# Optimization experiments

Measured on AMD Instinct MI355X. Metric: run time of the kernel, lower is better.

## Reference

```python
import jax, jax.numpy as jnp
import numpy as np

REACH = 3  # neighborhood reach -> 24 causal neighbors, 48 MLP input features


def setup_inputs() -> dict:
    key = jax.random.key(0)
    ks = jax.random.split(key, 5)
    b, c, h, w = 8, 3, 192, 192
    x = jax.random.uniform(ks[0], (b, c, h, w), dtype=jnp.float32)

    def lin(k, fi, fo):
        k1, k2 = jax.random.split(k)
        s = 1.0 / np.sqrt(fi).astype(np.float32)
        W = jax.random.uniform(k1, (fi, fo), minval=-s, maxval=s, dtype=jnp.float32)
        bias = jax.random.uniform(k2, (fo,), minval=-s, maxval=s, dtype=jnp.float32)
        return W, bias

    W1, b1 = lin(ks[1], 48, 96)
    W2, b2 = lin(ks[2], 96, 24)
    W3, b3 = lin(ks[3], 24, 12)
    W4, b4 = lin(ks[4], 12, 1)
    return dict(x=x, W1=W1, b1=b1, W2=W2, b2=b2, W3=W3, b3=b3, W4=W4, b4=b4)


def _forward(x, W1, b1, W2, b2, W3, b3, W4, b4):
    b, c, h, w = x.shape
    r = REACH
    H2, Wd = h - 2 * r, w - 2 * r  # interior grid of predicted pixels

    # Precompute the 24 image-neighborhood taps for every interior pixel.
    # Order matches torch get_nb: 3 rows above (7 cols each, row-major), then 3 cols left.
    slabs = [x[:, :, dy:dy + H2, dx:dx + Wd] for dy in range(r) for dx in range(2 * r + 1)]
    slabs += [x[:, :, r:r + H2, dx:dx + Wd] for dx in range(r)]
    xnb = jnp.transpose(jnp.stack(slabs, axis=-1), (2, 3, 0, 1, 4))   # (H2, Wd, b, c, 24)
    xtgt = jnp.transpose(x[:, :, r:r + H2, r:r + Wd], (2, 3, 0, 1))    # (H2, Wd, b, c)

    def mlp(f):  # f: (b, c, 48)
        f = jnp.tanh(f @ W1 + b1)
        f = jnp.tanh(f @ W2 + b2)
        f = jnp.tanh(f @ W3 + b3)
        f = jnp.tanh(f @ W4 + b4)
        return f[..., 0]  # (b, c)

    def row_step(prev3, row_xs):
        # prev3: (b, c, 3, w) = last 3 full (zero-padded) delta rows
        xnb_row, xtgt_row = row_xs  # (Wd, b, c, 24), (Wd, b, c)
        # 21 delta taps from the 3 previous rows, vectorized over columns.
        pslabs = [prev3[:, :, dy, dx:dx + Wd] for dy in range(r) for dx in range(2 * r + 1)]
        pnb = jnp.transpose(jnp.stack(pslabs, axis=-1), (2, 0, 1, 3))  # (Wd, b, c, 21)

        def col_step(last3, xs):
            # last3: (b, c, 3) = 3 most recent deltas in current row (zeros at row start)
            xn, pn, tgt = xs
            feat = jnp.concatenate([xn, pn, last3], axis=-1)  # (b, c, 48)
            delta = tgt - mlp(feat)
            last3 = jnp.concatenate([last3[:, :, 1:], delta[:, :, None]], axis=-1)
            return last3, delta

        last3_0 = jnp.zeros((b, c, r), x.dtype)
        _, row_d = jax.lax.scan(col_step, last3_0, (xnb_row, pnb, xtgt_row))  # (Wd, b, c)
        row_full = jnp.pad(jnp.transpose(row_d, (1, 2, 0)), ((0, 0), (0, 0), (r, w - r - Wd)))
        prev3 = jnp.concatenate([prev3[:, :, 1:, :], row_full[:, :, None, :]], axis=2)
        return prev3, row_d

    prev3_0 = jnp.zeros((b, c, r, w), x.dtype)
    _, all_d = jax.lax.scan(row_step, prev3_0, (xnb, xtgt))  # (H2, Wd, b, c)

    # torch averages square(deltas) over the full (b, c, h-2, w) buffer, whose
    # only nonzeros are the (H2, Wd) interior deltas.
    total = b * c * (h - 2) * w
    return jnp.sqrt(jnp.sum(all_d * all_d) / total)


def reference(x, W1, b1, W2, b2, W3, b3, W4, b4):
    return _forward(x, W1, b1, W2, b2, W3, b3, W4, b4)
```

## Files before the change

kernel.cpp:

```cpp
#include <hip/hip_runtime.h>

#define NPLANES 24
#define IMG 192
#define RW 194
#define GRID2 186
#define NPIX (GRID2 * GRID2)
#define SLACK 6
#define TSTEPS (926 + 11 * SLACK)

typedef _Float16 f16x8 __attribute__((ext_vector_type(8)));
typedef _Float16 h2v   __attribute__((ext_vector_type(2)));
typedef float    f32x4 __attribute__((ext_vector_type(4)));
typedef __fp16   fp16x2 __attribute__((ext_vector_type(2)));

__device__ float PreBuf[(unsigned long long)NPLANES * NPIX * 100];

__device__ __forceinline__ h2v pk(float a, float b) {
  union { fp16x2 p; h2v h; } u;
  u.p = __builtin_amdgcn_cvt_pkrtz(a, b);
  return u.h;
}
__device__ __forceinline__ unsigned pkn(float a, float b) {
  union { _Float16 h[2]; unsigned u; } x;
  x.h[0] = (_Float16)a; x.h[1] = (_Float16)b;
  return x.u;
}
__device__ __forceinline__ float fast_tanh(float x) {
  float e = __builtin_amdgcn_exp2f(x * 2.885390081777927f);
  return __builtin_fmaf(-2.0f, __builtin_amdgcn_rcpf(e + 1.0f), 1.0f);
}

__launch_bounds__(192)
__global__ void prepass_kernel(const float* __restrict__ x,
                               const float* __restrict__ W1g,
                               const float* __restrict__ b1g)
{
  __shared__ float xs[4][IMG];
  const int tid = threadIdx.x;
  const int plane = blockIdx.x / GRID2;
  const int a = blockIdx.x - plane * GRID2;
  const float* __restrict__ xp = x + (size_t)plane * (IMG * IMG) + (size_t)a * IMG;
  #pragma unroll
  for (int r = 0; r < 4; ++r) xs[r][tid] = xp[r * IMG + tid];
  __syncthreads();
  if (tid >= GRID2) return;

  float f[24];
  #pragma unroll
  for (int dy = 0; dy < 3; ++dy)
    #pragma unroll
    for (int dx = 0; dx < 7; ++dx) f[7 * dy + dx] = xs[dy][tid + dx];
  #pragma unroll
  for (int dx = 0; dx < 3; ++dx) f[21 + dx] = xs[3][tid + dx];

  float acc[96];
  #pragma unroll
  for (int n = 0; n < 96; ++n) acc[n] = b1g[n];
  #pragma unroll
  for (int k = 0; k < 24; ++k) {
    const float fk = f[k];
    const float* __restrict__ wr = W1g + k * 96;
    #pragma unroll
    for (int n = 0; n < 96; ++n) acc[n] = fmaf(fk, wr[n], acc[n]);
  }

  float* op = PreBuf + (size_t)(plane * NPIX + a * GRID2 + tid) * 100;
  #pragma unroll
  for (int g = 0; g < 4; ++g)
    #pragma unroll
    for (int nt = 0; nt < 6; ++nt) {
      float4 st;
      st.x = acc[32 * (nt >> 1) + 8 * g + 4 * (nt & 1) + 0];
      st.y = acc[32 * (nt >> 1) + 8 * g + 4 * (nt & 1) + 1];
      st.z = acc[32 * (nt >> 1) + 8 * g + 4 * (nt & 1) + 2];
      st.w = acc[32 * (nt >> 1) + 8 * g + 4 * (nt & 1) + 3];
      *(float4*)(op + g * 24 + nt * 4) = st;
    }
  op[96] = xs[3][tid + 3];
}

__launch_bounds__(192)
__global__ void codec_kernel(const float* __restrict__ x,
                             const float* __restrict__ W1g, const float* __restrict__ b1g,
                             const float* __restrict__ W2g, const float* __restrict__ b2g,
                             const float* __restrict__ W3g, const float* __restrict__ b3g,
                             const float* __restrict__ W4g, const float* __restrict__ b4g,
                             float* __restrict__ ws)
{
  __shared__ __align__(16) _Float16 ringH[64 * RW];
  __shared__ int   ctrL[4];
  __shared__ float wsum[3];

  const int tid  = threadIdx.x;
  const int lane = tid & 63;
  const int w    = __builtin_amdgcn_readfirstlane(tid >> 6);
  const int lam  = lane & 15;
  const int quad = lane >> 4;
  const int cell = 16 * w + lam;
  const float* __restrict__ pre = PreBuf + (size_t)blockIdx.x * NPIX * 100;
  (void)x; (void)b1g;

  { unsigned* z = (unsigned*)ringH; for (int u = tid; u < 64 * RW / 2; u += 192) z[u] = 0; }
  if (tid < 4) ctrL[tid] = -1;

  f16x8 A1s[6];
  #pragma unroll
  for (int nt = 0; nt < 6; ++nt) {
    union { _Float16 h[8]; f16x8 v; } u;
    const int n1 = 32 * (nt >> 1) + 8 * (lam >> 2) + 4 * (nt & 1) + (lam & 3);
    #pragma unroll
    for (int e = 0; e < 8; ++e) {
      float v = 0.f;
      if (quad == 0) {
        if (e < 2) v = W1g[(46 - e) * 96 + n1];
      } else if (quad == 1) {
        if (e < 6) v = W1g[(38 + e) * 96 + n1];
      } else if (e < 7) {
        v = W1g[(24 + 7 * (3 - quad) + e) * 96 + n1];
      }
      u.h[e] = (_Float16)v;
    }
    A1s[nt] = u.v;
  }
  f16x8 A1f[6];
  #pragma unroll
  for (int nt = 0; nt < 6; ++nt) {
    union { _Float16 h[8]; f16x8 v; } u;
    const int n1 = 32 * (nt >> 1) + 8 * (lam >> 2) + 4 * (nt & 1) + (lam & 3);
    #pragma unroll
    for (int e = 0; e < 8; ++e) {
      float v = 0.f;
      if (quad == 0 && e < 2) v = W1g[((e == 0) ? 44 : 47) * 96 + n1];
      u.h[e] = (_Float16)v;
    }
    A1f[nt] = u.v;
  }
  f16x8 A2[2][3];
  #pragma unroll
  for (int mt = 0; mt < 2; ++mt) {
    const int n2 = 8 * (lam >> 2) + 4 * mt + (lam & 3);
    #pragma unroll
    for (int kt = 0; kt < 3; ++kt) {
      union { _Float16 h[8]; f16x8 v; } u;
      #pragma unroll
      for (int e = 0; e < 8; ++e) {
        const int k2 = 32 * kt + 8 * quad + e;
        u.h[e] = (n2 < 24) ? (_Float16)W2g[k2 * 24 + n2] : (_Float16)0.f;
      }
      A2[mt][kt] = u.v;
    }
  }
  f16x8 A3;
  { union { _Float16 h[8]; f16x8 v; } u;
    #pragma unroll
    for (int e = 0; e < 8; ++e) {
      const int k3 = 8 * quad + e;
      u.h[e] = (k3 < 24 && lam < 12) ? (_Float16)W3g[k3 * 12 + lam] : (_Float16)0.f;
    }
    A3 = u.v; }
  f16x8 A4;
  { union { _Float16 h[8]; f16x8 v; } u;
    #pragma unroll
    for (int e = 0; e < 8; ++e) {
      const int m = 4 * quad + e;
      u.h[e] = ((lam & 3) == 0 && e < 4 && m < 12) ? (_Float16)W4g[m] : (_Float16)0.f;
    }
    A4 = u.v; }

  f32x4 b2q[2], b3q, b4q;
  #pragma unroll
  for (int mt = 0; mt < 2; ++mt)
    #pragma unroll
    for (int r = 0; r < 4; ++r) {
      const int n2 = 8 * quad + 4 * mt + r;
      b2q[mt][r] = (n2 < 24) ? b2g[n2] : 0.f;
    }
  #pragma unroll
  for (int r = 0; r < 4; ++r)
    b3q[r] = (4 * quad + r < 12) ? b3g[4 * quad + r] : 0.f;
  { const float b4v = b4g[0]; b4q[0] = b4v; b4q[1] = b4v; b4q[2] = b4v; b4q[3] = b4v; }

  __syncthreads();

  const int prodw = (w == 0) ? 2 : w - 1;
  const unsigned flagRA = (unsigned)(size_t)&ctrL[prodw];
  const unsigned flagWA = (unsigned)(size_t)&ctrL[w];
  const unsigned* ru32 = (const unsigned*)ringH;
  const unsigned short* rhu = (const unsigned short*)ringH;

  int i  = cell;
  int jj = -(4 * cell + SLACK * w);
  unsigned dl1g = 0, dl2g = 0;
  unsigned bfx0 = 0;
  float sumsq = 0.f, xtA = 0.f, xtB = 0.f;
  f32x4 SA[6], SB[6], PreP[6];
  #pragma unroll
  for (int q = 0; q < 6; ++q) {
    SA[q] = (f32x4){0.f,0.f,0.f,0.f};
    SB[q] = (f32x4){0.f,0.f,0.f,0.f};
    PreP[q] = (f32x4){0.f,0.f,0.f,0.f};
  }

  {
    if (jj >= 0 && i <= 185) {
      const float* pp = pre + (size_t)(i * GRID2 + jj) * 100;
      const f32x4* pv = (const f32x4*)(pp + quad * 24);
      #pragma unroll
      for (int q = 0; q < 6; ++q) PreP[q] = pv[q];
      xtA = pp[96];
    }
    const int rq = quad ? quad : 3;
    const int e0 = jj & ~1;
    const int dwi = ((i - rq) & 63) * 97 + (e0 >> 1);
    const unsigned w0 = ru32[dwi], w1 = ru32[dwi + 1];
    const unsigned w2 = ru32[dwi + 2], w3 = ru32[dwi + 3];
    const bool odd = jj & 1;
    const unsigned a01 = (w0 >> 16) | (w1 << 16);
    const unsigned a12 = (w1 >> 16) | (w2 << 16);
    const unsigned a23 = (w2 >> 16) | (w3 << 16);
    const unsigned t0 = odd ? a01 : w0, t1 = odd ? a12 : w1;
    const unsigned t2 = odd ? a23 : w2, t3 = odd ? (w3 >> 16) : w3;
    union { unsigned u[4]; f16x8 v; } bs;
    bs.u[0] = quad ? t0 : 0u;
    bs.u[1] = quad ? t1 : 0u;
    bs.u[2] = quad ? t2 : 0u;
    bs.u[3] = quad ? t3 : 0u;
    #pragma unroll
    for (int nt = 0; nt < 6; ++nt)
      SA[nt] = __builtin_amdgcn_mfma_f32_16x16x32_f16(A1s[nt], bs.v, PreP[nt], 0, 0, 0);
  }

#define SUBSTEP(T, SC, SN, XTC, XTN)                                            \
  {                                                                             \
    int _cv;                                                                    \
    asm volatile("ds_read_b32 %0, %1" : "=v"(_cv) : "v"(flagRA));               \
    const bool _act = (jj >= 0) && (i <= 185);                                  \
    const int _cb = 3 + jj;                                                     \
    int _iN = i, _jN = jj + 1;                                                  \
    if (_jN > 185) { _iN += 48; _jN -= 192 + 3 * SLACK; }                       \
                       \
    const int _rq = quad ? quad : 3;                                            \
    const int _e0 = _jN & ~1;                                                   \
    const int _dwi = ((_iN - _rq) & 63) * 97 + (_e0 >> 1);                      \
    const unsigned _w0 = ru32[_dwi],     _w1 = ru32[_dwi + 1];                  \
    const unsigned _w2 = ru32[_dwi + 2], _w3 = ru32[_dwi + 3];                  \
    const unsigned short _lf = rhu[((_iN - 1) & 63) * RW + (_jN + 6)];          \
    const unsigned _q0d = dl1g | (dl2g << 16);                                  \
    if (_jN >= 0 && _iN <= 185) {                                               \
      const float* _pp = pre + (size_t)(_iN * GRID2 + _jN) * 100;               \
      const f32x4* _pv = (const f32x4*)(_pp + quad * 24);                       \
      PreP[0]=_pv[0]; PreP[1]=_pv[1]; PreP[2]=_pv[2];                           \
      PreP[3]=_pv[3]; PreP[4]=_pv[4]; PreP[5]=_pv[5];                           \
      XTN = _pp[96];                                                            \
    }                                                                           \
                                      \
    union { unsigned u[4]; f16x8 v; } _bfx;                                     \
    _bfx.u[0] = bfx0; _bfx.u[1] = 0u; _bfx.u[2] = 0u; _bfx.u[3] = 0u;           \
    f32x4 _h1a[6];                                                              \
    _Pragma("unroll")                                                           \
    for (int nt = 0; nt < 6; ++nt)                                              \
      _h1a[nt] = __builtin_amdgcn_mfma_f32_16x16x32_f16(A1f[nt], _bfx.v, SC[nt], 0, 0, 0); \
    f16x8 _B2f[3];                                                              \
    _Pragma("unroll")                                                           \
    for (int kt = 0; kt < 3; ++kt) {                                            \
      union { h2v p[4]; f16x8 v; } _u;                                          \
      _u.p[0] = pk(fast_tanh(_h1a[2*kt][0]), fast_tanh(_h1a[2*kt][1]));         \
      _u.p[1] = pk(fast_tanh(_h1a[2*kt][2]), fast_tanh(_h1a[2*kt][3]));         \
      _u.p[2] = pk(fast_tanh(_h1a[2*kt+1][0]), fast_tanh(_h1a[2*kt+1][1]));     \
      _u.p[3] = pk(fast_tanh(_h1a[2*kt+1][2]), fast_tanh(_h1a[2*kt+1][3]));     \
      _B2f[kt] = _u.v;                                                          \
    }                                                                           \
    f32x4 _a20 = b2q[0], _a21 = b2q[1];                                         \
    _a20 = __builtin_amdgcn_mfma_f32_16x16x32_f16(A2[0][0], _B2f[0], _a20, 0, 0, 0); \
    _a20 = __builtin_amdgcn_mfma_f32_16x16x32_f16(A2[0][1], _B2f[1], _a20, 0, 0, 0); \
    _a20 = __builtin_amdgcn_mfma_f32_16x16x32_f16(A2[0][2], _B2f[2], _a20, 0, 0, 0); \
    _a21 = __builtin_amdgcn_mfma_f32_16x16x32_f16(A2[1][0], _B2f[0], _a21, 0, 0, 0); \
    _a21 = __builtin_amdgcn_mfma_f32_16x16x32_f16(A2[1][1], _B2f[1], _a21, 0, 0, 0); \
    _a21 = __builtin_amdgcn_mfma_f32_16x16x32_f16(A2[1][2], _B2f[2], _a21, 0, 0, 0); \
    f16x8 _B3f;                                                                 \
    { union { h2v p[4]; f16x8 v; } _u;                                          \
      _u.p[0] = pk(fast_tanh(_a20[0]), fast_tanh(_a20[1]));                     \
      _u.p[1] = pk(fast_tanh(_a20[2]), fast_tanh(_a20[3]));                     \
      _u.p[2] = pk(fast_tanh(_a21[0]), fast_tanh(_a21[1]));                     \
      _u.p[3] = pk(fast_tanh(_a21[2]), fast_tanh(_a21[3]));                     \
      _B3f = _u.v; }                                                            \
    f32x4 _a3 = __builtin_amdgcn_mfma_f32_16x16x32_f16(A3, _B3f, b3q, 0, 0, 0); \
    f16x8 _B4f;                                                                 \
    { union { unsigned u[4]; f16x8 v; } _u;                                     \
      union { h2v p; unsigned s; } _p0, _p1;                                    \
      _p0.p = pk(fast_tanh(_a3[0]), fast_tanh(_a3[1]));                         \
      _p1.p = pk(fast_tanh(_a3[2]), fast_tanh(_a3[3]));                         \
      _u.u[0] = _p0.s; _u.u[1] = _p1.s; _u.u[2] = 0u; _u.u[3] = 0u;             \
      _B4f = _u.v; }                                                            \
    const f32x4 _a4 = __builtin_amdgcn_mfma_f32_16x16x32_f16(A4, _B4f, b4q, 0, 0, 0); \
    const float _pred = fast_tanh(_a4[0]);                                      \
    const float _d = XTC - _pred;                                               \
    const float _de = _act ? _d : 0.f;                                          \
    if (quad == 0) sumsq += _de * _de;                                          \
    if (quad == 0 && _act) ringH[(i & 63) * RW + _cb] = (_Float16)_de;          \
             \
    { union { float f; int b; } _dc; _dc.f = _de;                               \
      int _si = __builtin_amdgcn_update_dpp(0, _dc.b, 0x111, 0xF, 0xF, false);  \
      union { int b; float f; } _sc; _sc.b = _si;                               \
      float _fr = _sc.f;                                                        \
      union { unsigned short s; _Float16 h; } _lh; _lh.s = _lf;                 \
      if (lam == 0) _fr = (float)_lh.h;                                         \
      if (_jN + 3 > 185) _fr = 0.f;                                             \
      bfx0 = (quad == 0) ? pkn(_fr, _de) : 0u; }                                \
                                \
    { union { _Float16 h; unsigned short s; } _dh; _dh.h = (_Float16)_de;       \
      if (_act) {                                                               \
        if (jj == 185) { dl1g = 0; dl2g = 0; }                                  \
        else { dl2g = dl1g; dl1g = (unsigned)_dh.s; }                           \
      } }                                                                       \
                                            \
    { const bool _odd = _jN & 1;                                                \
      const unsigned _a01 = (_w0 >> 16) | (_w1 << 16);                          \
      const unsigned _a12 = (_w1 >> 16) | (_w2 << 16);                          \
      const unsigned _a23 = (_w2 >> 16) | (_w3 << 16);                          \
      const unsigned _t0 = _odd ? _a01 : _w0, _t1 = _odd ? _a12 : _w1;          \
      const unsigned _t2 = _odd ? _a23 : _w2, _t3 = _odd ? (_w3 >> 16) : _w3;   \
      union { unsigned u[4]; f16x8 v; } _bs;                                    \
      _bs.u[0] = quad ? _t0 : _q0d;                                             \
      _bs.u[1] = quad ? _t1 : 0u;                                               \
      _bs.u[2] = quad ? _t2 : 0u;                                               \
      _bs.u[3] = quad ? _t3 : 0u;                                               \
      _Pragma("unroll")                                                         \
      for (int nt = 0; nt < 6; ++nt)                                            \
        SN[nt] = __builtin_amdgcn_mfma_f32_16x16x32_f16(A1s[nt], _bs.v, PreP[nt], 0, 0, 0); \
    }                                                                           \
        \
    if (lane == 0)                                                              \
      asm volatile("s_waitcnt lgkmcnt(0)\n\tds_write_b32 %0, %1"                \
                   :: "v"(flagWA), "v"(T) : "memory");                          \
    asm volatile("s_waitcnt lgkmcnt(0)" : "+v"(_cv) :: "memory");               \
    if (_cv < (T) - (SLACK - 1)) {                                              \
      int _g = 0;                                                               \
      do { __builtin_amdgcn_s_sleep(2);                                         \
           _cv = __hip_atomic_load(&ctrL[prodw], __ATOMIC_ACQUIRE,              \
                                   __HIP_MEMORY_SCOPE_WORKGROUP);               \
      } while (_cv < (T) - (SLACK - 1) && ++_g < (1 << 22));                    \
    }                                                                           \
    asm volatile("" ::: "memory");                                              \
    i = _iN; jj = _jN;                                                          \
  }

  for (int t = 0; t < TSTEPS; t += 2) {
    SUBSTEP(t,     SA, SB, xtA, xtB);
    SUBSTEP(t + 1, SB, SA, xtB, xtA);
  }
#undef SUBSTEP

  #pragma unroll
  for (int off = 32; off >= 1; off >>= 1) sumsq += __shfl_down(sumsq, off);
  if (lane == 0) wsum[w] = sumsq;
  __syncthreads();
  if (tid == 0) ws[blockIdx.x] = wsum[0] + wsum[1] + wsum[2];
}

__global__ void finalize_kernel(const float* __restrict__ ws, float* __restrict__ out) {
  if (threadIdx.x == 0) {
    float s = 0.0f;
    #pragma unroll
    for (int p = 0; p < NPLANES; ++p) s += ws[p];
    out[0] = sqrtf(s / 875520.0f);
  }
}

extern "C" void kernel_launch(void* const* d_in, const int* in_sizes, int n_in,
                              void* d_out, int out_size, void* d_ws, size_t ws_size,
                              hipStream_t stream) {
  (void)in_sizes; (void)n_in; (void)out_size; (void)ws_size;
  const float* x  = (const float*)d_in[0];
  const float* W1 = (const float*)d_in[1];
  const float* b1 = (const float*)d_in[2];
  const float* W2 = (const float*)d_in[3];
  const float* b2 = (const float*)d_in[4];
  const float* W3 = (const float*)d_in[5];
  const float* b3 = (const float*)d_in[6];
  const float* W4 = (const float*)d_in[7];
  const float* b4 = (const float*)d_in[8];
  float* ws = (float*)d_ws;

  prepass_kernel<<<NPLANES * GRID2, 192, 0, stream>>>(x, W1, b1);
  codec_kernel<<<NPLANES, 192, 0, stream>>>(x, W1, b1, W2, b2, W3, b3, W4, b4, ws);
  finalize_kernel<<<1, 64, 0, stream>>>(ws, (float*)d_out);
}
```

Measured before the change: 1.235 ms.

## Pack two planes per block and use four waves per plane in codec

The sequential codec kernel now runs two image planes per workgroup, and each plane gets four wavefronts instead of three. Each wave still owns 16 rows in the wavefront-skewed schedule, so a pass now covers 64 rows and the row-wrap offsets are updated to match. This halves the number of workgroups and adds a wave per plane, keeping the total step count unchanged. The aim is more latency hiding per CU, at the cost of eight waves competing for the same CU's SIMDs and a longer producer–consumer chain per plane.

```diff
diff --git a/kernel.cpp b/kernel.cpp
--- a/kernel.cpp
+++ b/kernel.cpp
@@ -7,6 +7,10 @@
 #define NPIX (GRID2 * GRID2)
 #define SLACK 6
 #define TSTEPS (926 + 11 * SLACK)
+#define PPB 2
+#define WPP 4
+#define NTHR (PPB * WPP * 64)
+#define NBLK (NPLANES / PPB)
 
 typedef _Float16 f16x8 __attribute__((ext_vector_type(8)));
 typedef _Float16 h2v   __attribute__((ext_vector_type(2)));
@@ -79,7 +83,7 @@
   op[96] = xs[3][tid + 3];
 }
 
-__launch_bounds__(192)
+__launch_bounds__(NTHR)
 __global__ void codec_kernel(const float* __restrict__ x,
                              const float* __restrict__ W1g, const float* __restrict__ b1g,
                              const float* __restrict__ W2g, const float* __restrict__ b2g,
@@ -87,21 +91,26 @@
                              const float* __restrict__ W4g, const float* __restrict__ b4g,
                              float* __restrict__ ws)
 {
-  __shared__ __align__(16) _Float16 ringH[64 * RW];
-  __shared__ int   ctrL[4];
-  __shared__ float wsum[3];
+  __shared__ __align__(16) _Float16 ringS[PPB][64 * RW];
+  __shared__ int   ctrL[PPB][4];
+  __shared__ float wsum[PPB][WPP];
 
   const int tid  = threadIdx.x;
   const int lane = tid & 63;
-  const int w    = __builtin_amdgcn_readfirstlane(tid >> 6);
+  const int Wv   = __builtin_amdgcn_readfirstlane(tid >> 6);
+  const int pl   = Wv >> 2;
+  const int w    = Wv & 3;
   const int lam  = lane & 15;
   const int quad = lane >> 4;
   const int cell = 16 * w + lam;
-  const float* __restrict__ pre = PreBuf + (size_t)blockIdx.x * NPIX * 100;
+  const int ptid = tid & (NTHR / PPB - 1);
+  const int plane = blockIdx.x * PPB + pl;
+  const float* __restrict__ pre = PreBuf + (size_t)plane * NPIX * 100;
+  _Float16* __restrict__ ringH = ringS[pl];
   (void)x; (void)b1g;
 
-  { unsigned* z = (unsigned*)ringH; for (int u = tid; u < 64 * RW / 2; u += 192) z[u] = 0; }
-  if (tid < 4) ctrL[tid] = -1;
+  { unsigned* z = (unsigned*)ringH; for (int u = ptid; u < 64 * RW / 2; u += 256) z[u] = 0; }
+  if (ptid < 4) ctrL[pl][ptid] = -1;
 
   f16x8 A1s[6];
   #pragma unroll
@@ -182,11 +191,11 @@
 
   __syncthreads();
 
-  const int prodw = (w == 0) ? 2 : w - 1;
-  const unsigned flagRA = (unsigned)(size_t)&ctrL[prodw];
-  const unsigned flagWA = (unsigned)(size_t)&ctrL[w];
+  const unsigned flagRA = (unsigned)(size_t)&ctrL[pl][(w + 3) & 3];
+  const unsigned flagWA = (unsigned)(size_t)&ctrL[pl][w];
   const unsigned* ru32 = (const unsigned*)ringH;
   const unsigned short* rhu = (const unsigned short*)ringH;
+  int* const prodCtr = &ctrL[pl][(w + 3) & 3];
 
   int i  = cell;
   int jj = -(4 * cell + SLACK * w);
@@ -237,7 +246,7 @@
     const bool _act = (jj >= 0) && (i <= 185);                                  \
     const int _cb = 3 + jj;                                                     \
     int _iN = i, _jN = jj + 1;                                                  \
-    if (_jN > 185) { _iN += 48; _jN -= 192 + 3 * SLACK; }                       \
+    if (_jN > 185) { _iN += 64; _jN -= 256 + 4 * SLACK; }                       \
                        \
     const int _rq = quad ? quad : 3;                                            \
     const int _e0 = _jN & ~1;                                                   \
@@ -307,7 +316,7 @@
       if (lam == 0) _fr = (float)_lh.h;                                         \
       if (_jN + 3 > 185) _fr = 0.f;                                             \
       bfx0 = (quad == 0) ? pkn(_fr, _de) : 0u; }                                \
-                                \
+                                                            \
     { union { _Float16 h; unsigned short s; } _dh; _dh.h = (_Float16)_de;       \
       if (_act) {                                                               \
         if (jj == 185) { dl1g = 0; dl2g = 0; }                                  \
@@ -337,7 +346,7 @@
     if (_cv < (T) - (SLACK - 1)) {                                              \
       int _g = 0;                                                               \
       do { __builtin_amdgcn_s_sleep(2);                                         \
-           _cv = __hip_atomic_load(&ctrL[prodw], __ATOMIC_ACQUIRE,              \
+           _cv = __hip_atomic_load(prodCtr, __ATOMIC_ACQUIRE,                   \
                                    __HIP_MEMORY_SCOPE_WORKGROUP);               \
       } while (_cv < (T) - (SLACK - 1) && ++_g < (1 << 22));                    \
     }                                                                           \
@@ -353,9 +362,10 @@
 
   #pragma unroll
   for (int off = 32; off >= 1; off >>= 1) sumsq += __shfl_down(sumsq, off);
-  if (lane == 0) wsum[w] = sumsq;
+  if (lane == 0) wsum[pl][w] = sumsq;
   __syncthreads();
-  if (tid == 0) ws[blockIdx.x] = wsum[0] + wsum[1] + wsum[2];
+  if (ptid == 0)
+    ws[plane] = wsum[pl][0] + wsum[pl][1] + wsum[pl][2] + wsum[pl][3];
 }
 
 __global__ void finalize_kernel(const float* __restrict__ ws, float* __restrict__ out) {
@@ -383,6 +393,6 @@
   float* ws = (float*)d_ws;
 
   prepass_kernel<<<NPLANES * GRID2, 192, 0, stream>>>(x, W1, b1);
-  codec_kernel<<<NPLANES, 192, 0, stream>>>(x, W1, b1, W2, b2, W3, b3, W4, b4, ws);
+  codec_kernel<<<NBLK, NTHR, 0, stream>>>(x, W1, b1, W2, b2, W3, b3, W4, b4, ws);
   finalize_kernel<<<1, 64, 0, stream>>>(ws, (float*)d_out);
 }
```

After: 1.650 ms. 33.6% more time.

## Batch tanh reciprocals, reduce wavefront slack, and move progress flag after wait

Applied to the files above, without the earlier changes.

Adds a tanh4 helper that computes four tanh values with a single shared reciprocal, replacing four separate rcp ops per accumulator vector. The pipeline slack between producer and consumer waves drops from 6 to 4, which shortens the total step count. The progress-flag write now happens after the spin-wait instead of before it. That shortens the serial dependence chain, but it changes the publish ordering and can lose precision or overflow when the exp products are large.

```diff
diff --git a/kernel.cpp b/kernel.cpp
--- a/kernel.cpp
+++ b/kernel.cpp
@@ -5,7 +5,7 @@
 #define RW 194
 #define GRID2 186
 #define NPIX (GRID2 * GRID2)
-#define SLACK 6
+#define SLACK 4
 #define TSTEPS (926 + 11 * SLACK)
 
 typedef _Float16 f16x8 __attribute__((ext_vector_type(8)));
@@ -28,6 +28,22 @@
 __device__ __forceinline__ float fast_tanh(float x) {
   float e = __builtin_amdgcn_exp2f(x * 2.885390081777927f);
   return __builtin_fmaf(-2.0f, __builtin_amdgcn_rcpf(e + 1.0f), 1.0f);
+}
+__device__ __forceinline__ f32x4 tanh4(f32x4 x) {
+  const float K = 2.885390081777927f;
+  const float a0 = __builtin_amdgcn_exp2f(x[0] * K) + 1.0f;
+  const float a1 = __builtin_amdgcn_exp2f(x[1] * K) + 1.0f;
+  const float a2 = __builtin_amdgcn_exp2f(x[2] * K) + 1.0f;
+  const float a3 = __builtin_amdgcn_exp2f(x[3] * K) + 1.0f;
+  const float q01 = a0 * a1, q23 = a2 * a3;
+  const float r = __builtin_amdgcn_rcpf(q01 * q23);
+  const float r01 = r * q23, r23 = r * q01;
+  f32x4 o;
+  o[0] = __builtin_fmaf(-2.0f, r01 * a1, 1.0f);
+  o[1] = __builtin_fmaf(-2.0f, r01 * a0, 1.0f);
+  o[2] = __builtin_fmaf(-2.0f, r23 * a3, 1.0f);
+  o[3] = __builtin_fmaf(-2.0f, r23 * a2, 1.0f);
+  return o;
 }
 
 __launch_bounds__(192)
@@ -187,6 +203,7 @@
   const unsigned flagWA = (unsigned)(size_t)&ctrL[w];
   const unsigned* ru32 = (const unsigned*)ringH;
   const unsigned short* rhu = (const unsigned short*)ringH;
+  int* const prodCtr = &ctrL[prodw];
 
   int i  = cell;
   int jj = -(4 * cell + SLACK * w);
@@ -263,11 +280,13 @@
     f16x8 _B2f[3];                                                              \
     _Pragma("unroll")                                                           \
     for (int kt = 0; kt < 3; ++kt) {                                            \
+      const f32x4 _ta = tanh4(_h1a[2 * kt]);                                    \
+      const f32x4 _tb = tanh4(_h1a[2 * kt + 1]);                                \
       union { h2v p[4]; f16x8 v; } _u;                                          \
-      _u.p[0] = pk(fast_tanh(_h1a[2*kt][0]), fast_tanh(_h1a[2*kt][1]));         \
-      _u.p[1] = pk(fast_tanh(_h1a[2*kt][2]), fast_tanh(_h1a[2*kt][3]));         \
-      _u.p[2] = pk(fast_tanh(_h1a[2*kt+1][0]), fast_tanh(_h1a[2*kt+1][1]));     \
-      _u.p[3] = pk(fast_tanh(_h1a[2*kt+1][2]), fast_tanh(_h1a[2*kt+1][3]));     \
+      _u.p[0] = pk(_ta[0], _ta[1]);                                             \
+      _u.p[1] = pk(_ta[2], _ta[3]);                                             \
+      _u.p[2] = pk(_tb[0], _tb[1]);                                             \
+      _u.p[3] = pk(_tb[2], _tb[3]);                                             \
       _B2f[kt] = _u.v;                                                          \
     }                                                                           \
     f32x4 _a20 = b2q[0], _a21 = b2q[1];                                         \
@@ -278,18 +297,22 @@
     _a21 = __builtin_amdgcn_mfma_f32_16x16x32_f16(A2[1][1], _B2f[1], _a21, 0, 0, 0); \
     _a21 = __builtin_amdgcn_mfma_f32_16x16x32_f16(A2[1][2], _B2f[2], _a21, 0, 0, 0); \
     f16x8 _B3f;                                                                 \
-    { union { h2v p[4]; f16x8 v; } _u;                                          \
-      _u.p[0] = pk(fast_tanh(_a20[0]), fast_tanh(_a20[1]));                     \
-      _u.p[1] = pk(fast_tanh(_a20[2]), fast_tanh(_a20[3]));                     \
-      _u.p[2] = pk(fast_tanh(_a21[0]), fast_tanh(_a21[1]));                     \
-      _u.p[3] = pk(fast_tanh(_a21[2]), fast_tanh(_a21[3]));                     \
+    { const f32x4 _ta = tanh4(_a20);                                            \
+      const f32x4 _tb = tanh4(_a21);                                            \
+      union { h2v p[4]; f16x8 v; } _u;                                          \
+      _u.p[0] = pk(_ta[0], _ta[1]);                                             \
+      _u.p[1] = pk(_ta[2], _ta[3]);                                             \
+      _u.p[2] = pk(_tb[0], _tb[1]);                                             \
+      _u.p[3] = pk(_tb[2], _tb[3]);                                             \
       _B3f = _u.v; }                                                            \
     f32x4 _a3 = __builtin_amdgcn_mfma_f32_16x16x32_f16(A3, _B3f, b3q, 0, 0, 0); \
     f16x8 _B4f;                                                                 \
-    { union { unsigned u[4]; f16x8 v; } _u;                                     \
+    { const f32x4 _t3 = tanh4(_a3);                                             \
+      union { unsigned u[4]; f16x8 v; } _u;                                     \
+      _u.u[0] = pkn(0.f, 0.f);                                                  \
       union { h2v p; unsigned s; } _p0, _p1;                                    \
-      _p0.p = pk(fast_tanh(_a3[0]), fast_tanh(_a3[1]));                         \
-      _p1.p = pk(fast_tanh(_a3[2]), fast_tanh(_a3[3]));                         \
+      _p0.p = pk(_t3[0], _t3[1]);                                               \
+      _p1.p = pk(_t3[2], _t3[3]);                                               \
       _u.u[0] = _p0.s; _u.u[1] = _p1.s; _u.u[2] = 0u; _u.u[3] = 0u;             \
       _B4f = _u.v; }                                                            \
     const f32x4 _a4 = __builtin_amdgcn_mfma_f32_16x16x32_f16(A4, _B4f, b4q, 0, 0, 0); \
@@ -307,7 +330,7 @@
       if (lam == 0) _fr = (float)_lh.h;                                         \
       if (_jN + 3 > 185) _fr = 0.f;                                             \
       bfx0 = (quad == 0) ? pkn(_fr, _de) : 0u; }                                \
-                                \
+                                                            \
     { union { _Float16 h; unsigned short s; } _dh; _dh.h = (_Float16)_de;       \
       if (_act) {                                                               \
         if (jj == 185) { dl1g = 0; dl2g = 0; }                                  \
@@ -329,18 +352,17 @@
       for (int nt = 0; nt < 6; ++nt)                                            \
         SN[nt] = __builtin_amdgcn_mfma_f32_16x16x32_f16(A1s[nt], _bs.v, PreP[nt], 0, 0, 0); \
     }                                                                           \
-        \
-    if (lane == 0)                                                              \
-      asm volatile("s_waitcnt lgkmcnt(0)\n\tds_write_b32 %0, %1"                \
-                   :: "v"(flagWA), "v"(T) : "memory");                          \
+     \
     asm volatile("s_waitcnt lgkmcnt(0)" : "+v"(_cv) :: "memory");               \
     if (_cv < (T) - (SLACK - 1)) {                                              \
       int _g = 0;                                                               \
       do { __builtin_amdgcn_s_sleep(2);                                         \
-           _cv = __hip_atomic_load(&ctrL[prodw], __ATOMIC_ACQUIRE,              \
+           _cv = __hip_atomic_load(prodCtr, __ATOMIC_ACQUIRE,                   \
                                    __HIP_MEMORY_SCOPE_WORKGROUP);               \
       } while (_cv < (T) - (SLACK - 1) && ++_g < (1 << 22));                    \
     }                                                                           \
+    if (lane == 0)                                                              \
+      asm volatile("ds_write_b32 %0, %1" :: "v"(flagWA), "v"(T) : "memory");    \
     asm volatile("" ::: "memory");                                              \
     i = _iN; jj = _jN;                                                          \
   }
```

Result: no change. 1.249 ms (+1.1%).
